# Performance work log

Measured on AMD Instinct MI355X. Metric: run time of the kernel, lower is better.

## Reference

```python
import jax, jax.numpy as jnp
import numpy as np

B, N, C, H, W = 16, 8, 3, 48, 48
K = 5          # kernel_size=[5]
NK = 4         # hardcoded multi-kernel weight groups in the module


def setup_inputs() -> dict:
    key = jax.random.key(0)
    k1, k2, k3 = jax.random.split(key, 3)
    frames = jax.random.normal(k1, (B, N, C, H, W), jnp.float32)
    # core as produced by _convert_dict: [B, N, K*K, 3, 4, H, W]
    core = jax.random.normal(k2, (B, N, K * K, C, NK, H, W), jnp.float32)
    kernel_weight = jax.random.normal(k3, (B, N, NK, C, H, W), jnp.float32)
    return {"frames": frames, "core": core, "kernel_weight": kernel_weight}


def reference(frames, core, kernel_weight):
    b, n, c, h, w = frames.shape
    kk = K * K
    # torch: padded_kernel = stack([core[5]], dim=2) -> [B,N,1,25,3,4,H,W]
    #        .view(B, N, 4, -1, 3, 48, 48): row-major reinterpretation of the
    #        flattened (25*3*4)=300 middle dims into (4, 25, 3).
    pk = core.reshape(b, n, NK, kk, c, h, w)
    # kernel_weight.unsqueeze(3) -> [B,N,4,1,3,H,W]; mean over the 4 groups
    wk = jnp.mean(pk * kernel_weight[:, :, :, None], axis=2)  # [B,N,25,3,H,W]
    # im2col-style gather: pad by K//2 and stack the 25 spatial shifts
    p = K // 2
    fp = jnp.pad(frames, ((0, 0), (0, 0), (0, 0), (p, p), (p, p)))
    img_stack = jnp.stack(
        [fp[..., i:i + h, j:j + w] for i in range(K) for j in range(K)],
        axis=2,
    )  # [B,N,25,3,H,W]
    # pred_rgb[i] = sum_k sum_c wk[:,:,k,i] * img_stack[:,:,k,c]
    frames_sum = jnp.sum(img_stack, axis=3)  # [B,N,25,H,W]
    pred_img_i = jnp.einsum('bnkihw,bnkhw->bnihw', wk, frames_sum)  # [B,N,3,H,W]
    pred_img = jnp.mean(pred_img_i, axis=1)  # [B,3,H,W]
    return pred_img_i, pred_img
```

## Files before the change

### kernel.cpp

```cpp
#include <hip/hip_runtime.h>
#include <stdint.h>
#include <stddef.h>

constexpr int B_ = 16, N_ = 8, C_ = 3, H_ = 48, W_ = 48, K_ = 5, NK_ = 4;
constexpr int HW_ = H_ * W_;
constexpr int IMGS_ = B_ * N_;
constexpr int CHUNKS_ = HW_ / 256;
constexpr int TW_ = 52;
constexpr int TH_ = 10;

typedef float f32x4 __attribute__((ext_vector_type(4)));

__global__ __launch_bounds__(256) void kmain(const float* __restrict__ frames,
                                             const float* __restrict__ core,
                                             const float* __restrict__ kw,
                                             float* __restrict__ out) {
    __shared__ float tile[TH_][TW_];
    __shared__ float red[4][4][64];

    int t = threadIdx.x;
    int q = t & 63;
    int g = t >> 6;
    int bx = blockIdx.x;
    int c = bx % 3;
    int ic = bx / 3;
    int img = ic / CHUNKS_;
    int chunk = ic - img * CHUNKS_;
    int pix0 = chunk * 256 + q * 4;
    int h = pix0 / W_;
    int w0 = pix0 - h * W_;
    int r0 = (chunk * 256) / W_;

    const float* fb = frames + (size_t)img * (C_ * HW_);
    for (int i = t; i < TH_ * TW_; i += 256) {
        int pr = i / TW_;
        int pc = i - pr * TW_;
        int hh = r0 + pr - 2, ww = pc - 2;
        float s = 0.f;
        if ((unsigned)hh < (unsigned)H_ && (unsigned)ww < (unsigned)W_) {
            const float* f = fb + hh * W_ + ww;
            s = f[0] + f[HW_] + f[2 * HW_];
        }
        tile[pr][pc] = s;
    }
    __syncthreads();

    float fs[5][8];
#pragma unroll
    for (int rr = 0; rr < 5; ++rr) {
        f32x4 a = *(const f32x4*)&tile[h - r0 + rr][w0];
        f32x4 b = *(const f32x4*)&tile[h - r0 + rr][w0 + 4];
        fs[rr][0] = a.x; fs[rr][1] = a.y; fs[rr][2] = a.z; fs[rr][3] = a.w;
        fs[rr][4] = b.x; fs[rr][5] = b.y; fs[rr][6] = b.z; fs[rr][7] = b.w;
    }

    const float* cp = core + (size_t)img * (300 * HW_)
                           + (size_t)(g * 75 + c) * HW_ + pix0;

    float t0 = 0.f, t1 = 0.f, t2 = 0.f, t3 = 0.f;
#pragma unroll
    for (int k = 0; k < 25; ++k) {
        f32x4 d = __builtin_nontemporal_load((const f32x4*)(cp + (size_t)(k * 3) * HW_));
        int di = k / 5, dj = k - di * 5;
        t0 += d.x * fs[di][dj + 0];
        t1 += d.y * fs[di][dj + 1];
        t2 += d.z * fs[di][dj + 2];
        t3 += d.w * fs[di][dj + 3];
    }
    f32x4 kd = __builtin_nontemporal_load(
        (const f32x4*)(kw + (size_t)img * (12 * HW_) + (size_t)(g * 3 + c) * HW_ + pix0));
    red[g][0][q] = kd.x * t0;
    red[g][1][q] = kd.y * t1;
    red[g][2][q] = kd.z * t2;
    red[g][3][q] = kd.w * t3;

    __syncthreads();

    if (t < 64) {
        f32x4 o;
#pragma unroll
        for (int j = 0; j < 4; ++j) {
            o[j] = 0.25f * (red[0][j][t] + red[1][j][t] + red[2][j][t] + red[3][j][t]);
        }
        *(f32x4*)(out + (size_t)img * (3 * HW_) + (size_t)c * HW_ + chunk * 256 + t * 4) = o;
    }
}

__global__ void kmean(const float* __restrict__ outi, float* __restrict__ outm) {
    int id = blockIdx.x * blockDim.x + threadIdx.x;
    if (id >= B_ * 3 * HW_) return;
    int b = id / (3 * HW_);
    int rem = id - b * (3 * HW_);
    const float* p = outi + (size_t)b * (N_ * 3 * HW_) + rem;
    float s = 0.f;
#pragma unroll
    for (int n = 0; n < N_; ++n) s += p[(size_t)n * 3 * HW_];
    outm[id] = s * 0.125f;
}

extern "C" void kernel_launch(void* const* d_in, const int* in_sizes, int n_in,
                              void* d_out, int out_size, void* d_ws, size_t ws_size,
                              hipStream_t stream) {
    const float* frames = (const float*)d_in[0];
    const float* core = (const float*)d_in[1];
    const float* kw = (const float*)d_in[2];
    float* outi = (float*)d_out;
    float* outm = outi + (size_t)B_ * N_ * 3 * HW_;

    kmain<<<IMGS_ * CHUNKS_ * 3, 256, 0, stream>>>(frames, core, kw, outi);
    kmean<<<(B_ * 3 * HW_ + 255) / 256, 256, 0, stream>>>(outi, outm);
}
```

Measured before the change: 448.0 us.

## Restructure main kernel to one block per image-group with partial-sum reduction pass

The main kernel now launches one 576-thread block per (image, weight group). Each block loads the full padded frame-sum tile and walks all 75 contiguous core planes, computing all three colour channels per thread. Group partials are written to workspace, and a new reduction kernel averages the four groups. The per-block shared-memory reduction goes away and the tile setup is amortised over more work, but the change costs an extra kernel launch, a round trip through workspace memory, and fewer, larger blocks.

```diff
diff --git a/kernel.cpp b/kernel.cpp
--- a/kernel.cpp
+++ b/kernel.cpp
@@ -5,37 +5,26 @@
 constexpr int B_ = 16, N_ = 8, C_ = 3, H_ = 48, W_ = 48, K_ = 5, NK_ = 4;
 constexpr int HW_ = H_ * W_;
 constexpr int IMGS_ = B_ * N_;
-constexpr int CHUNKS_ = HW_ / 256;
-constexpr int TW_ = 52;
-constexpr int TH_ = 10;
+constexpr int TP_ = 52;
 
 typedef float f32x4 __attribute__((ext_vector_type(4)));
 
-__global__ __launch_bounds__(256) void kmain(const float* __restrict__ frames,
+__global__ __launch_bounds__(576) void kmain(const float* __restrict__ frames,
                                              const float* __restrict__ core,
                                              const float* __restrict__ kw,
-                                             float* __restrict__ out) {
-    __shared__ float tile[TH_][TW_];
-    __shared__ float red[4][4][64];
+                                             float* __restrict__ part) {
+    __shared__ float tile[TP_][TP_];
 
     int t = threadIdx.x;
-    int q = t & 63;
-    int g = t >> 6;
     int bx = blockIdx.x;
-    int c = bx % 3;
-    int ic = bx / 3;
-    int img = ic / CHUNKS_;
-    int chunk = ic - img * CHUNKS_;
-    int pix0 = chunk * 256 + q * 4;
-    int h = pix0 / W_;
-    int w0 = pix0 - h * W_;
-    int r0 = (chunk * 256) / W_;
+    int img = bx >> 2;
+    int g = bx & 3;
 
     const float* fb = frames + (size_t)img * (C_ * HW_);
-    for (int i = t; i < TH_ * TW_; i += 256) {
-        int pr = i / TW_;
-        int pc = i - pr * TW_;
-        int hh = r0 + pr - 2, ww = pc - 2;
+    for (int i = t; i < TP_ * TP_; i += 576) {
+        int pr = i / TP_;
+        int pc = i - pr * TP_;
+        int hh = pr - 2, ww = pc - 2;
         float s = 0.f;
         if ((unsigned)hh < (unsigned)H_ && (unsigned)ww < (unsigned)W_) {
             const float* f = fb + hh * W_ + ww;
@@ -45,45 +34,60 @@
     }
     __syncthreads();
 
+    int px0 = t * 4;
+    int h0 = px0 / W_;
+    int w0 = px0 - h0 * W_;
+
     float fs[5][8];
 #pragma unroll
     for (int rr = 0; rr < 5; ++rr) {
-        f32x4 a = *(const f32x4*)&tile[h - r0 + rr][w0];
-        f32x4 b = *(const f32x4*)&tile[h - r0 + rr][w0 + 4];
+        f32x4 a = *(const f32x4*)&tile[h0 + rr][w0];
+        f32x4 b = *(const f32x4*)&tile[h0 + rr][w0 + 4];
         fs[rr][0] = a.x; fs[rr][1] = a.y; fs[rr][2] = a.z; fs[rr][3] = a.w;
         fs[rr][4] = b.x; fs[rr][5] = b.y; fs[rr][6] = b.z; fs[rr][7] = b.w;
     }
 
-    const float* cp = core + (size_t)img * (300 * HW_)
-                           + (size_t)(g * 75 + c) * HW_ + pix0;
+    const float* cp = core + ((size_t)img * 300 + (size_t)g * 75) * HW_ + px0;
+    float acc[3][4] = {{0.f, 0.f, 0.f, 0.f}, {0.f, 0.f, 0.f, 0.f}, {0.f, 0.f, 0.f, 0.f}};
+#pragma unroll
+    for (int p = 0; p < 75; ++p) {
+        f32x4 d = __builtin_nontemporal_load((const f32x4*)(cp + (size_t)p * HW_));
+        int k = p / 3;
+        int c = p - k * 3;
+        int di = k / 5, dj = k - di * 5;
+        acc[c][0] += d.x * fs[di][dj + 0];
+        acc[c][1] += d.y * fs[di][dj + 1];
+        acc[c][2] += d.z * fs[di][dj + 2];
+        acc[c][3] += d.w * fs[di][dj + 3];
+    }
 
-    float t0 = 0.f, t1 = 0.f, t2 = 0.f, t3 = 0.f;
+    const float* kp = kw + (size_t)img * (12 * HW_) + (size_t)(g * 3) * HW_ + px0;
+    float* pp = part + ((size_t)(img * 4 + g) * 3) * HW_ + px0;
 #pragma unroll
-    for (int k = 0; k < 25; ++k) {
-        f32x4 d = __builtin_nontemporal_load((const f32x4*)(cp + (size_t)(k * 3) * HW_));
-        int di = k / 5, dj = k - di * 5;
-        t0 += d.x * fs[di][dj + 0];
-        t1 += d.y * fs[di][dj + 1];
-        t2 += d.z * fs[di][dj + 2];
-        t3 += d.w * fs[di][dj + 3];
+    for (int c = 0; c < 3; ++c) {
+        f32x4 kd = __builtin_nontemporal_load((const f32x4*)(kp + (size_t)c * HW_));
+        f32x4 o;
+        o.x = acc[c][0] * kd.x;
+        o.y = acc[c][1] * kd.y;
+        o.z = acc[c][2] * kd.z;
+        o.w = acc[c][3] * kd.w;
+        *(f32x4*)(pp + (size_t)c * HW_) = o;
     }
-    f32x4 kd = __builtin_nontemporal_load(
-        (const f32x4*)(kw + (size_t)img * (12 * HW_) + (size_t)(g * 3 + c) * HW_ + pix0));
-    red[g][0][q] = kd.x * t0;
-    red[g][1][q] = kd.y * t1;
-    red[g][2][q] = kd.z * t2;
-    red[g][3][q] = kd.w * t3;
+}
 
-    __syncthreads();
-
-    if (t < 64) {
-        f32x4 o;
-#pragma unroll
-        for (int j = 0; j < 4; ++j) {
-            o[j] = 0.25f * (red[0][j][t] + red[1][j][t] + red[2][j][t] + red[3][j][t]);
-        }
-        *(f32x4*)(out + (size_t)img * (3 * HW_) + (size_t)c * HW_ + chunk * 256 + t * 4) = o;
-    }
+__global__ void kred(const float* __restrict__ part, float* __restrict__ outi) {
+    int id = blockIdx.x * blockDim.x + threadIdx.x;
+    if (id >= IMGS_ * 3 * HW_ / 4) return;
+    int img = id / (3 * HW_ / 4);
+    int rem = id - img * (3 * HW_ / 4);
+    size_t off = (size_t)rem * 4;
+    const float* p0 = part + (size_t)img * (12 * HW_) + off;
+    f32x4 a = *(const f32x4*)(p0);
+    f32x4 b = *(const f32x4*)(p0 + 3 * HW_);
+    f32x4 c = *(const f32x4*)(p0 + 6 * HW_);
+    f32x4 d = *(const f32x4*)(p0 + 9 * HW_);
+    f32x4 o = (a + b + c + d) * 0.25f;
+    *(f32x4*)(outi + (size_t)img * (3 * HW_) + off) = o;
 }
 
 __global__ void kmean(const float* __restrict__ outi, float* __restrict__ outm) {
@@ -104,9 +108,11 @@
     const float* frames = (const float*)d_in[0];
     const float* core = (const float*)d_in[1];
     const float* kw = (const float*)d_in[2];
+    float* part = (float*)d_ws;
     float* outi = (float*)d_out;
     float* outm = outi + (size_t)B_ * N_ * 3 * HW_;
 
-    kmain<<<IMGS_ * CHUNKS_ * 3, 256, 0, stream>>>(frames, core, kw, outi);
+    kmain<<<IMGS_ * NK_, 576, 0, stream>>>(frames, core, kw, part);
+    kred<<<(IMGS_ * 3 * HW_ / 4 + 255) / 256, 256, 0, stream>>>(part, outi);
     kmean<<<(B_ * 3 * HW_ + 255) / 256, 256, 0, stream>>>(outi, outm);
 }
```

After: 458.1 us. 1.02x slower.
